# Optimization experiments

Measured on AMD Instinct MI355X. Metric: run time of the kernel, lower is better.

## Reference

```python
import jax, jax.numpy as jnp
import numpy as np

N_NODES = 50000
EMBED_DIM = 128
N_EDGES = 500000


def setup_inputs() -> dict:
    key = jax.random.key(0)
    k_x, k_e, k_w1, k_w2 = jax.random.split(key, 4)
    s = 1.0 / np.sqrt(EMBED_DIM)
    return {
        "x": jax.random.normal(k_x, (N_NODES, EMBED_DIM), dtype=jnp.float32),
        "edge_index": jax.random.randint(k_e, (2, N_EDGES), 0, N_NODES, dtype=jnp.int64),
        "W1": jax.random.normal(k_w1, (EMBED_DIM, EMBED_DIM), dtype=jnp.float32) * s,
        "b1": jnp.zeros((EMBED_DIM,), dtype=jnp.float32),
        "W2": jax.random.normal(k_w2, (EMBED_DIM, EMBED_DIM), dtype=jnp.float32) * s,
        "b2": jnp.zeros((EMBED_DIM,), dtype=jnp.float32),
    }


def _gcn_conv(x, src, dst, norm, W, b, n_nodes):
    # PyG GCNConv: h = x @ W; out[i] = sum_{j->i} norm_e * h[j] + b
    h = x @ W                              # [N, D] small GEMM
    msg = h[src] * norm[:, None]           # gather + scale, [E+N, D]
    out = jax.ops.segment_sum(msg, dst, num_segments=n_nodes)
    return out + b


def reference(x, edge_index, W1, b1, W2, b2):
    n = x.shape[0]
    # add self loops (GCNConv default add_self_loops=True)
    loop = jnp.arange(n, dtype=edge_index.dtype)
    src = jnp.concatenate([edge_index[0], loop])
    dst = jnp.concatenate([edge_index[1], loop])
    # symmetric normalization: deg over destination (in-degree incl. self loop)
    deg = jax.ops.segment_sum(jnp.ones_like(src, dtype=x.dtype), dst, num_segments=n)
    dis = jnp.where(deg > 0, jax.lax.rsqrt(jnp.maximum(deg, 1e-12)), 0.0)
    norm = dis[src] * dis[dst]             # [E+N]

    init_embeds = x  # Identity init embedding
    h = jnp.tanh(_gcn_conv(init_embeds, src, dst, norm, W1, b1, n))
    h = jnp.tanh(_gcn_conv(h, src, dst, norm, W2, b2, n))
    return (h, init_embeds)
```

## Files before the change

kernel.cpp:

```cpp
#include <hip/hip_runtime.h>

#define D 128
#define CAP 64
#define EPB 2048

typedef short bf16x8 __attribute__((ext_vector_type(8)));
typedef float f32x4  __attribute__((ext_vector_type(4)));
typedef float f32x2  __attribute__((ext_vector_type(2)));

__device__ __forceinline__ unsigned f2bf(float f) {
    unsigned u = __float_as_uint(f);
    return (u + 0x7fffu + ((u >> 16) & 1u)) >> 16;
}

__global__ __launch_bounds__(256) void k_pre(
    const float* __restrict__ W1, const float* __restrict__ W2,
    ushort* __restrict__ Wt1, ushort* __restrict__ Wt2,
    const int* __restrict__ ei, int* __restrict__ cnt, ushort* __restrict__ ewsrc,
    uint* __restrict__ Xf8, uint* __restrict__ H1f8,
    int ne, int nch, int N, int slabN) {
    const int blk = blockIdx.x, t = threadIdx.x;
    if (blk < nch * 8) {
        const int chunk = blk >> 3;
        const int slab = blk & 7;
        const int lo = slab * slabN;
        const int hi = min(lo + slabN, N);
        const int base = chunk * EPB;
        const int lim = min(base + EPB, ne);
        for (int e = base + t; e < lim; e += 256) {
            int d = ei[ne + e];
            if (d >= lo && d < hi) {
                int s = ei[e];
                int sl = atomicAdd(&cnt[d], 1);
                if (sl < CAP - 1) ewsrc[(uint)d * CAP + sl] = (ushort)s;
            }
        }
    } else {
        if (blk == nch * 8) {
            if (t < 32) Xf8[(size_t)N * 32 + t] = 0;
            else if (t < 64) H1f8[(size_t)N * 32 + (t - 32)] = 0;
        }
        int i = (blk - nch * 8) * 256 + t;
        const float* W = (i < D * D) ? W1 : W2;
        ushort* Wt = (i < D * D) ? Wt1 : Wt2;
        int j = i & (D * D - 1);
        int nn = j >> 7, k = j & 127;
        Wt[nn * 128 + k] = (ushort)f2bf(W[k * 128 + nn]);
    }
}

__global__ __launch_bounds__(256) void k_scale(
    const float4* __restrict__ x4, float4* __restrict__ out2,
    const int* __restrict__ cnt,
    uint* __restrict__ Xf8, ushort* __restrict__ ewsrc, int n4, int N) {
    int i = blockIdx.x * 256 + threadIdx.x;
    if (i < n4) {
        float4 v = x4[i];
        out2[i] = v;
        float s = rsqrtf((float)cnt[i >> 5] + 1.0f);
        uint q = __builtin_amdgcn_cvt_pk_fp8_f32(v.x * s, v.y * s, 0, false);
        q = __builtin_amdgcn_cvt_pk_fp8_f32(v.z * s, v.w * s, q, true);
        Xf8[i] = q;
    }
    if (i < N) {
        int dg = cnt[i]; if (dg > CAP - 1) dg = CAP - 1;
        int pd = (dg + 4) & ~3;
        ushort* r = ewsrc + (uint)i * CAP;
        r[dg] = (ushort)i;
        for (int p = dg + 1; p < pd; ++p) r[p] = (ushort)N;
    }
}

template <bool FP8OUT>
__global__ __launch_bounds__(256) void k_layer(
    const int* __restrict__ cnt, const ushort* __restrict__ ewsrc,
    const uint* __restrict__ Ain8, const ushort* __restrict__ Wt,
    const float* __restrict__ bias, void* __restrict__ out, int n, int nsent) {
    __shared__ ushort atile[16 * 136];
    __shared__ float otile[16 * 132];
    const int wid = threadIdx.x >> 6;
    const int lane = threadIdx.x & 63;
    const int fl = lane & 31;
    const int half = lane >> 5;
    const uint sentw = ((uint)nsent) | (((uint)nsent) << 16);
    const int base = blockIdx.x * 16;

    int nd[4], pdeg[4]; float di[4]; int maxp = 0;
#pragma unroll
    for (int j = 0; j < 4; ++j) {
        int node = base + wid * 4 + j;
        bool ok = node < n;
        int dg = ok ? cnt[node] : 0;
        di[j] = __builtin_amdgcn_rsqf((float)dg + 1.0f);
        if (dg > CAP - 1) dg = CAP - 1;
        nd[j] = ok ? node : nsent;
        pdeg[j] = ok ? ((dg + 4) & ~3) : 4;
        maxp = max(maxp, pdeg[j]);
    }
    f32x2 aL[4], aH[4];
#pragma unroll
    for (int j = 0; j < 4; ++j) { aL[j] = (f32x2){0.f, 0.f}; aH[j] = (f32x2){0.f, 0.f}; }

    uint4 qA[4], qB[4];
#pragma unroll
    for (int j = 0; j < 4; ++j) {
        const uint4* rs4 = (const uint4*)(ewsrc + (uint)nd[j] * CAP);
        qA[j] = rs4[0];
        qB[j] = rs4[1];
    }
#pragma unroll
    for (int j = 0; j < 4; ++j) {
        if (pdeg[j] <= 4)  { qA[j].z = sentw; qA[j].w = sentw; }
        if (pdeg[j] <= 8)  { qB[j].x = sentw; qB[j].y = sentw; }
        if (pdeg[j] <= 12) { qB[j].z = sentw; qB[j].w = sentw; }
    }

#define LOAD8(u, qx, qy)                                             \
    {                                                                \
        uint r0 = half ? ((qx).x >> 16) : ((qx).x & 0xffffu);        \
        uint r1 = half ? ((qx).y >> 16) : ((qx).y & 0xffffu);        \
        uint r2 = half ? ((qx).z >> 16) : ((qx).z & 0xffffu);        \
        uint r3 = half ? ((qx).w >> 16) : ((qx).w & 0xffffu);        \
        uint r4 = half ? ((qy).x >> 16) : ((qy).x & 0xffffu);        \
        uint r5 = half ? ((qy).y >> 16) : ((qy).y & 0xffffu);        \
        uint r6 = half ? ((qy).z >> 16) : ((qy).z & 0xffffu);        \
        uint r7 = half ? ((qy).w >> 16) : ((qy).w & 0xffffu);        \
        u[0] = Ain8[r0 * 32 + fl]; u[1] = Ain8[r1 * 32 + fl];        \
        u[2] = Ain8[r2 * 32 + fl]; u[3] = Ain8[r3 * 32 + fl];        \
        u[4] = Ain8[r4 * 32 + fl]; u[5] = Ain8[r5 * 32 + fl];        \
        u[6] = Ain8[r6 * 32 + fl]; u[7] = Ain8[r7 * 32 + fl];        \
    }

#define CONS8(u, j0)                                                      \
    {                                                                     \
        f32x2 l0 = __builtin_amdgcn_cvt_pk_f32_fp8(u[0], false);          \
        f32x2 h0 = __builtin_amdgcn_cvt_pk_f32_fp8(u[0], true);           \
        f32x2 l1 = __builtin_amdgcn_cvt_pk_f32_fp8(u[1], false);          \
        f32x2 h1 = __builtin_amdgcn_cvt_pk_f32_fp8(u[1], true);           \
        f32x2 l2 = __builtin_amdgcn_cvt_pk_f32_fp8(u[2], false);          \
        f32x2 h2 = __builtin_amdgcn_cvt_pk_f32_fp8(u[2], true);           \
        f32x2 l3 = __builtin_amdgcn_cvt_pk_f32_fp8(u[3], false);          \
        f32x2 h3 = __builtin_amdgcn_cvt_pk_f32_fp8(u[3], true);           \
        aL[j0] += (l0 + l1) + (l2 + l3);                                  \
        aH[j0] += (h0 + h1) + (h2 + h3);                                  \
        f32x2 m0 = __builtin_amdgcn_cvt_pk_f32_fp8(u[4], false);          \
        f32x2 g0 = __builtin_amdgcn_cvt_pk_f32_fp8(u[4], true);           \
        f32x2 m1 = __builtin_amdgcn_cvt_pk_f32_fp8(u[5], false);          \
        f32x2 g1 = __builtin_amdgcn_cvt_pk_f32_fp8(u[5], true);           \
        f32x2 m2 = __builtin_amdgcn_cvt_pk_f32_fp8(u[6], false);          \
        f32x2 g2 = __builtin_amdgcn_cvt_pk_f32_fp8(u[6], true);           \
        f32x2 m3 = __builtin_amdgcn_cvt_pk_f32_fp8(u[7], false);          \
        f32x2 g3 = __builtin_amdgcn_cvt_pk_f32_fp8(u[7], true);           \
        aL[j0 + 1] += (m0 + m1) + (m2 + m3);                              \
        aH[j0 + 1] += (g0 + g1) + (g2 + g3);                              \
    }

    {
        uint u0[8], u1[8], u2[8], u3[8];
        LOAD8(u0, qA[0], qA[1]);
        LOAD8(u1, qA[2], qA[3]);
        LOAD8(u2, qB[0], qB[1]);
        CONS8(u0, 0);
        LOAD8(u3, qB[2], qB[3]);
        CONS8(u1, 2);
        CONS8(u2, 0);
        CONS8(u3, 2);
    }

    if (maxp > 16) {
        for (int e = 16; e < maxp; e += 8) {
            uint4 qq[4];
#pragma unroll
            for (int j = 0; j < 4; ++j) {
                const ushort* rs = ewsrc + (uint)nd[j] * CAP + e;
                uint2 qa = *(const uint2*)(rs);
                uint2 qb = *(const uint2*)(rs + 4);
                if (e + 4 > pdeg[j]) { qa.x = sentw; qa.y = sentw; }
                if (e + 8 > pdeg[j]) { qb.x = sentw; qb.y = sentw; }
                qq[j] = make_uint4(qa.x, qa.y, qb.x, qb.y);
            }
            uint v0[8], v1[8];
            LOAD8(v0, qq[0], qq[1]);
            LOAD8(v1, qq[2], qq[3]);
            CONS8(v0, 0);
            CONS8(v1, 2);
        }
    }
#undef LOAD8
#undef CONS8

#pragma unroll
    for (int j = 0; j < 4; ++j) {
        float s0 = aL[j].x + __shfl_xor(aL[j].x, 32, 64);
        float s1 = aL[j].y + __shfl_xor(aL[j].y, 32, 64);
        float s2 = aH[j].x + __shfl_xor(aH[j].x, 32, 64);
        float s3 = aH[j].y + __shfl_xor(aH[j].y, 32, 64);
        if (half == 0) {
            s0 *= di[j]; s1 *= di[j]; s2 *= di[j]; s3 *= di[j];
            uint p0 = f2bf(s0) | (f2bf(s1) << 16);
            uint p1 = f2bf(s2) | (f2bf(s3) << 16);
            uint* arow = (uint*)atile + (wid * 4 + j) * 68;
            arow[2 * fl] = p0;
            arow[2 * fl + 1] = p1;
        }
    }
    __syncthreads();

    const int m = lane & 15, quad = lane >> 4;
    const ushort* ar = atile + m * 136 + quad * 8;
    bf16x8 afr[4];
#pragma unroll
    for (int kc = 0; kc < 4; ++kc) afr[kc] = *(const bf16x8*)(ar + kc * 32);

    f32x4 acc[2];
#pragma unroll
    for (int t2 = 0; t2 < 2; ++t2) {
        acc[t2] = (f32x4){0.f, 0.f, 0.f, 0.f};
        const int t = wid * 2 + t2;
        const ushort* wrow = Wt + (size_t)(t * 16 + m) * 128 + quad * 8;
#pragma unroll
        for (int kc = 0; kc < 4; ++kc) {
            bf16x8 b = *(const bf16x8*)(wrow + kc * 32);
            acc[t2] = __builtin_amdgcn_mfma_f32_16x16x32_bf16(afr[kc], b, acc[t2], 0, 0, 0);
        }
    }

#pragma unroll
    for (int t2 = 0; t2 < 2; ++t2) {
        const int t = wid * 2 + t2;
        float bb = bias[t * 16 + m];
#pragma unroll
        for (int r = 0; r < 4; ++r)
            otile[(quad * 4 + r) * 132 + t * 16 + m] = tanhf(acc[t2][r] + bb);
    }
    __syncthreads();

    const int row = threadIdx.x >> 4, seg = threadIdx.x & 15;
    if (base + row < n) {
        const float* src = &otile[row * 132 + seg * 8];
        if (FP8OUT) {
            float s = rsqrtf((float)cnt[base + row] + 1.0f);
            uint q0 = __builtin_amdgcn_cvt_pk_fp8_f32(src[0] * s, src[1] * s, 0, false);
            q0 = __builtin_amdgcn_cvt_pk_fp8_f32(src[2] * s, src[3] * s, q0, true);
            uint q1 = __builtin_amdgcn_cvt_pk_fp8_f32(src[4] * s, src[5] * s, 0, false);
            q1 = __builtin_amdgcn_cvt_pk_fp8_f32(src[6] * s, src[7] * s, q1, true);
            ((uint2*)out)[(size_t)(base + row) * 16 + seg] = make_uint2(q0, q1);
        } else {
            float4* dst = (float4*)((float*)out + (size_t)(base + row) * 128 + seg * 8);
            dst[0] = *(const float4*)(src);
            dst[1] = *(const float4*)(src + 4);
        }
    }
}

extern "C" void kernel_launch(void* const* d_in, const int* in_sizes, int n_in,
                              void* d_out, int out_size, void* d_ws, size_t ws_size,
                              hipStream_t stream) {
    const float* x  = (const float*)d_in[0];
    const int*   ei = (const int*)d_in[1];
    const float* W1 = (const float*)d_in[2];
    const float* b1 = (const float*)d_in[3];
    const float* W2 = (const float*)d_in[4];
    const float* b2 = (const float*)d_in[5];
    const int N = in_sizes[0] / D;
    const int E = in_sizes[1] / 2;
    float* out = (float*)d_out;

    char* ws = (char*)d_ws;
    const size_t KB = 1024, MB = 1024 * KB;
    int*    cnt   = (int*)(ws + 0);
    ushort* ewsrc = (ushort*)(ws + 1 * MB);
    uint*   Xf8   = (uint*)(ws + 8 * MB);
    uint*   H1f8  = (uint*)(ws + 16 * MB);
    ushort* Wt1   = (ushort*)(ws + 24 * MB);
    ushort* Wt2   = (ushort*)(ws + 24 * MB + 64 * KB);

    const int n4 = N * D / 4;
    const int nb = (n4 + 255) / 256;
    const int nch = (E + EPB - 1) / EPB;
    const int slabN = (N + 7) / 8;
    const int lblocks = (N + 15) / 16;

    hipMemsetAsync(cnt, 0, (size_t)(N + 1) * sizeof(int), stream);
    k_pre<<<nch * 8 + 128, 256, 0, stream>>>(
        W1, W2, Wt1, Wt2, ei, cnt, ewsrc, Xf8, H1f8, E, nch, N, slabN);
    k_scale<<<nb, 256, 0, stream>>>((const float4*)x, (float4*)(out + (size_t)N * D),
                                    cnt, Xf8, ewsrc, n4, N);

    k_layer<true><<<lblocks, 256, 0, stream>>>(cnt, ewsrc, Xf8, Wt1,
                                               b1, (void*)H1f8, N, N);
    k_layer<false><<<lblocks, 256, 0, stream>>>(cnt, ewsrc, H1f8, Wt2,
                                                b2, (void*)out, N, N);
}
```

Baseline: 177.9 us.

## Process 32 nodes per block in GCN layer kernel to reuse weight fragments

Each layer block now handles 32 destination nodes instead of 16. It gathers two groups of neighbor rows with more loads in flight and runs two MFMA row tiles against each loaded weight fragment. This halves the weight loads per node and raises memory-level parallelism in the gather. In exchange it uses more registers and LDS per block and launches half as many blocks, which may lower occupancy and load balance.

```diff
diff --git a/kernel.cpp b/kernel.cpp
--- a/kernel.cpp
+++ b/kernel.cpp
@@ -76,32 +76,36 @@
     const int* __restrict__ cnt, const ushort* __restrict__ ewsrc,
     const uint* __restrict__ Ain8, const ushort* __restrict__ Wt,
     const float* __restrict__ bias, void* __restrict__ out, int n, int nsent) {
-    __shared__ ushort atile[16 * 136];
-    __shared__ float otile[16 * 132];
+    __shared__ ushort atile[32 * 136];
+    __shared__ float otile[32 * 132];
     const int wid = threadIdx.x >> 6;
     const int lane = threadIdx.x & 63;
     const int fl = lane & 31;
     const int half = lane >> 5;
     const uint sentw = ((uint)nsent) | (((uint)nsent) << 16);
-    const int base = blockIdx.x * 16;
-
-    int nd[4], pdeg[4]; float di[4]; int maxp = 0;
-#pragma unroll
-    for (int j = 0; j < 4; ++j) {
-        int node = base + wid * 4 + j;
-        bool ok = node < n;
-        int dg = ok ? cnt[node] : 0;
-        di[j] = __builtin_amdgcn_rsqf((float)dg + 1.0f);
-        if (dg > CAP - 1) dg = CAP - 1;
-        nd[j] = ok ? node : nsent;
-        pdeg[j] = ok ? ((dg + 4) & ~3) : 4;
-        maxp = max(maxp, pdeg[j]);
-    }
-    f32x2 aL[4], aH[4];
-#pragma unroll
-    for (int j = 0; j < 4; ++j) { aL[j] = (f32x2){0.f, 0.f}; aH[j] = (f32x2){0.f, 0.f}; }
-
-    uint4 qA[4], qB[4];
+    const int base = blockIdx.x * 32;
+
+    int nd[8], pdeg[8]; float di[8]; int maxp0 = 0, maxp1 = 0;
+#pragma unroll
+    for (int g = 0; g < 2; ++g)
+#pragma unroll
+        for (int j = 0; j < 4; ++j) {
+            int idx = g * 4 + j;
+            int node = base + g * 16 + wid * 4 + j;
+            bool ok = node < n;
+            int dg = ok ? cnt[node] : 0;
+            di[idx] = __builtin_amdgcn_rsqf((float)dg + 1.0f);
+            if (dg > CAP - 1) dg = CAP - 1;
+            nd[idx] = ok ? node : nsent;
+            pdeg[idx] = ok ? ((dg + 4) & ~3) : 4;
+            if (g == 0) maxp0 = max(maxp0, pdeg[idx]);
+            else        maxp1 = max(maxp1, pdeg[idx]);
+        }
+    f32x2 aL[8], aH[8];
+#pragma unroll
+    for (int j = 0; j < 8; ++j) { aL[j] = (f32x2){0.f, 0.f}; aH[j] = (f32x2){0.f, 0.f}; }
+
+    uint4 qA[4], qB[4], qC[4], qD[4];
 #pragma unroll
     for (int j = 0; j < 4; ++j) {
         const uint4* rs4 = (const uint4*)(ewsrc + (uint)nd[j] * CAP);
@@ -110,9 +114,18 @@
     }
 #pragma unroll
     for (int j = 0; j < 4; ++j) {
+        const uint4* rs4 = (const uint4*)(ewsrc + (uint)nd[4 + j] * CAP);
+        qC[j] = rs4[0];
+        qD[j] = rs4[1];
+    }
+#pragma unroll
+    for (int j = 0; j < 4; ++j) {
         if (pdeg[j] <= 4)  { qA[j].z = sentw; qA[j].w = sentw; }
         if (pdeg[j] <= 8)  { qB[j].x = sentw; qB[j].y = sentw; }
         if (pdeg[j] <= 12) { qB[j].z = sentw; qB[j].w = sentw; }
+        if (pdeg[4 + j] <= 4)  { qC[j].z = sentw; qC[j].w = sentw; }
+        if (pdeg[4 + j] <= 8)  { qD[j].x = sentw; qD[j].y = sentw; }
+        if (pdeg[4 + j] <= 12) { qD[j].z = sentw; qD[j].w = sentw; }
     }
 
 #define LOAD8(u, qx, qy)                                             \
@@ -156,72 +169,89 @@
     }
 
     {
-        uint u0[8], u1[8], u2[8], u3[8];
+        uint u0[8], u1[8], u2[8], u3[8], v0[8], v1[8], v2[8], v3[8];
         LOAD8(u0, qA[0], qA[1]);
         LOAD8(u1, qA[2], qA[3]);
         LOAD8(u2, qB[0], qB[1]);
         CONS8(u0, 0);
         LOAD8(u3, qB[2], qB[3]);
         CONS8(u1, 2);
+        LOAD8(v0, qC[0], qC[1]);
         CONS8(u2, 0);
+        LOAD8(v1, qC[2], qC[3]);
         CONS8(u3, 2);
-    }
-
-    if (maxp > 16) {
-        for (int e = 16; e < maxp; e += 8) {
+        LOAD8(v2, qD[0], qD[1]);
+        CONS8(v0, 4);
+        LOAD8(v3, qD[2], qD[3]);
+        CONS8(v1, 6);
+        CONS8(v2, 4);
+        CONS8(v3, 6);
+    }
+
+    auto overflow = [&](int off, int mp) {
+        for (int e = 16; e < mp; e += 8) {
             uint4 qq[4];
 #pragma unroll
             for (int j = 0; j < 4; ++j) {
-                const ushort* rs = ewsrc + (uint)nd[j] * CAP + e;
+                const ushort* rs = ewsrc + (uint)nd[off + j] * CAP + e;
                 uint2 qa = *(const uint2*)(rs);
                 uint2 qb = *(const uint2*)(rs + 4);
-                if (e + 4 > pdeg[j]) { qa.x = sentw; qa.y = sentw; }
-                if (e + 8 > pdeg[j]) { qb.x = sentw; qb.y = sentw; }
+                if (e + 4 > pdeg[off + j]) { qa.x = sentw; qa.y = sentw; }
+                if (e + 8 > pdeg[off + j]) { qb.x = sentw; qb.y = sentw; }
                 qq[j] = make_uint4(qa.x, qa.y, qb.x, qb.y);
             }
-            uint v0[8], v1[8];
-            LOAD8(v0, qq[0], qq[1]);
-            LOAD8(v1, qq[2], qq[3]);
-            CONS8(v0, 0);
-            CONS8(v1, 2);
-        }
-    }
+            uint w0[8], w1[8];
+            LOAD8(w0, qq[0], qq[1]);
+            LOAD8(w1, qq[2], qq[3]);
+            CONS8(w0, off);
+            CONS8(w1, off + 2);
+        }
+    };
+    if (maxp0 > 16) overflow(0, maxp0);
+    if (maxp1 > 16) overflow(4, maxp1);
 #undef LOAD8
 #undef CONS8
 
 #pragma unroll
-    for (int j = 0; j < 4; ++j) {
-        float s0 = aL[j].x + __shfl_xor(aL[j].x, 32, 64);
-        float s1 = aL[j].y + __shfl_xor(aL[j].y, 32, 64);
-        float s2 = aH[j].x + __shfl_xor(aH[j].x, 32, 64);
-        float s3 = aH[j].y + __shfl_xor(aH[j].y, 32, 64);
-        if (half == 0) {
-            s0 *= di[j]; s1 *= di[j]; s2 *= di[j]; s3 *= di[j];
-            uint p0 = f2bf(s0) | (f2bf(s1) << 16);
-            uint p1 = f2bf(s2) | (f2bf(s3) << 16);
-            uint* arow = (uint*)atile + (wid * 4 + j) * 68;
-            arow[2 * fl] = p0;
-            arow[2 * fl + 1] = p1;
-        }
-    }
+    for (int g = 0; g < 2; ++g)
+#pragma unroll
+        for (int j = 0; j < 4; ++j) {
+            int idx = g * 4 + j;
+            float s0 = aL[idx].x + __shfl_xor(aL[idx].x, 32, 64);
+            float s1 = aL[idx].y + __shfl_xor(aL[idx].y, 32, 64);
+            float s2 = aH[idx].x + __shfl_xor(aH[idx].x, 32, 64);
+            float s3 = aH[idx].y + __shfl_xor(aH[idx].y, 32, 64);
+            if (half == 0) {
+                s0 *= di[idx]; s1 *= di[idx]; s2 *= di[idx]; s3 *= di[idx];
+                uint p0 = f2bf(s0) | (f2bf(s1) << 16);
+                uint p1 = f2bf(s2) | (f2bf(s3) << 16);
+                uint* arow = (uint*)atile + (g * 16 + wid * 4 + j) * 68;
+                arow[2 * fl] = p0;
+                arow[2 * fl + 1] = p1;
+            }
+        }
     __syncthreads();
 
     const int m = lane & 15, quad = lane >> 4;
-    const ushort* ar = atile + m * 136 + quad * 8;
-    bf16x8 afr[4];
-#pragma unroll
-    for (int kc = 0; kc < 4; ++kc) afr[kc] = *(const bf16x8*)(ar + kc * 32);
-
-    f32x4 acc[2];
+    bf16x8 afr0[4], afr1[4];
+#pragma unroll
+    for (int kc = 0; kc < 4; ++kc) {
+        afr0[kc] = *(const bf16x8*)(atile + m * 136 + quad * 8 + kc * 32);
+        afr1[kc] = *(const bf16x8*)(atile + (16 + m) * 136 + quad * 8 + kc * 32);
+    }
+
+    f32x4 acc[2][2];
 #pragma unroll
     for (int t2 = 0; t2 < 2; ++t2) {
-        acc[t2] = (f32x4){0.f, 0.f, 0.f, 0.f};
+        acc[0][t2] = (f32x4){0.f, 0.f, 0.f, 0.f};
+        acc[1][t2] = (f32x4){0.f, 0.f, 0.f, 0.f};
         const int t = wid * 2 + t2;
         const ushort* wrow = Wt + (size_t)(t * 16 + m) * 128 + quad * 8;
 #pragma unroll
         for (int kc = 0; kc < 4; ++kc) {
             bf16x8 b = *(const bf16x8*)(wrow + kc * 32);
-            acc[t2] = __builtin_amdgcn_mfma_f32_16x16x32_bf16(afr[kc], b, acc[t2], 0, 0, 0);
+            acc[0][t2] = __builtin_amdgcn_mfma_f32_16x16x32_bf16(afr0[kc], b, acc[0][t2], 0, 0, 0);
+            acc[1][t2] = __builtin_amdgcn_mfma_f32_16x16x32_bf16(afr1[kc], b, acc[1][t2], 0, 0, 0);
         }
     }
 
@@ -230,25 +260,31 @@
         const int t = wid * 2 + t2;
         float bb = bias[t * 16 + m];
 #pragma unroll
-        for (int r = 0; r < 4; ++r)
-            otile[(quad * 4 + r) * 132 + t * 16 + m] = tanhf(acc[t2][r] + bb);
+        for (int tl = 0; tl < 2; ++tl)
+#pragma unroll
+            for (int r = 0; r < 4; ++r)
+                otile[(tl * 16 + quad * 4 + r) * 132 + t * 16 + m] = tanhf(acc[tl][t2][r] + bb);
     }
     __syncthreads();
 
-    const int row = threadIdx.x >> 4, seg = threadIdx.x & 15;
-    if (base + row < n) {
-        const float* src = &otile[row * 132 + seg * 8];
-        if (FP8OUT) {
-            float s = rsqrtf((float)cnt[base + row] + 1.0f);
-            uint q0 = __builtin_amdgcn_cvt_pk_fp8_f32(src[0] * s, src[1] * s, 0, false);
-            q0 = __builtin_amdgcn_cvt_pk_fp8_f32(src[2] * s, src[3] * s, q0, true);
-            uint q1 = __builtin_amdgcn_cvt_pk_fp8_f32(src[4] * s, src[5] * s, 0, false);
-            q1 = __builtin_amdgcn_cvt_pk_fp8_f32(src[6] * s, src[7] * s, q1, true);
-            ((uint2*)out)[(size_t)(base + row) * 16 + seg] = make_uint2(q0, q1);
-        } else {
-            float4* dst = (float4*)((float*)out + (size_t)(base + row) * 128 + seg * 8);
-            dst[0] = *(const float4*)(src);
-            dst[1] = *(const float4*)(src + 4);
+    const int seg = threadIdx.x & 15;
+#pragma unroll
+    for (int r2 = 0; r2 < 2; ++r2) {
+        const int row = r2 * 16 + (threadIdx.x >> 4);
+        if (base + row < n) {
+            const float* src = &otile[row * 132 + seg * 8];
+            if (FP8OUT) {
+                float s = rsqrtf((float)cnt[base + row] + 1.0f);
+                uint q0 = __builtin_amdgcn_cvt_pk_fp8_f32(src[0] * s, src[1] * s, 0, false);
+                q0 = __builtin_amdgcn_cvt_pk_fp8_f32(src[2] * s, src[3] * s, q0, true);
+                uint q1 = __builtin_amdgcn_cvt_pk_fp8_f32(src[4] * s, src[5] * s, 0, false);
+                q1 = __builtin_amdgcn_cvt_pk_fp8_f32(src[6] * s, src[7] * s, q1, true);
+                ((uint2*)out)[(size_t)(base + row) * 16 + seg] = make_uint2(q0, q1);
+            } else {
+                float4* dst = (float4*)((float*)out + (size_t)(base + row) * 128 + seg * 8);
+                dst[0] = *(const float4*)(src);
+                dst[1] = *(const float4*)(src + 4);
+            }
         }
     }
 }
@@ -279,7 +315,7 @@
     const int nb = (n4 + 255) / 256;
     const int nch = (E + EPB - 1) / EPB;
     const int slabN = (N + 7) / 8;
-    const int lblocks = (N + 15) / 16;
+    const int lblocks = (N + 31) / 32;
 
     hipMemsetAsync(cnt, 0, (size_t)(N + 1) * sizeof(int), stream);
     k_pre<<<nch * 8 + 128, 256, 0, stream>>>(
```

New measurement: 175.9 us. About the same (-1.1%).
